# Performance work log

Measured on AMD Instinct MI355X. Metric: run time of the kernel, lower is better.

Reference implementation:

```python
import jax, jax.numpy as jnp
import numpy as np

INPUT_DIM = 1024
HIDDEN_DIM = 1024

def setup_inputs() -> dict:
    key = jax.random.key(0)
    ks = jax.random.split(key, 9)
    s_in = 1.0 / np.sqrt(INPUT_DIM)
    s_h = 1.0 / np.sqrt(HIDDEN_DIM)
    x = jax.random.normal(ks[0], (4, 2048, INPUT_DIM), dtype=jnp.float32)
    Wq = jax.random.uniform(ks[1], (INPUT_DIM, HIDDEN_DIM), jnp.float32, -s_in, s_in)
    bq = jax.random.uniform(ks[2], (HIDDEN_DIM,), jnp.float32, -s_in, s_in)
    Wk = jax.random.uniform(ks[3], (INPUT_DIM, HIDDEN_DIM), jnp.float32, -s_in, s_in)
    bk = jax.random.uniform(ks[4], (HIDDEN_DIM,), jnp.float32, -s_in, s_in)
    Wv = jax.random.uniform(ks[5], (INPUT_DIM, HIDDEN_DIM), jnp.float32, -s_in, s_in)
    bv = jax.random.uniform(ks[6], (HIDDEN_DIM,), jnp.float32, -s_in, s_in)
    Wo = jax.random.uniform(ks[7], (HIDDEN_DIM, INPUT_DIM), jnp.float32, -s_h, s_h)
    bo = jax.random.uniform(ks[8], (INPUT_DIM,), jnp.float32, -s_h, s_h)
    return {"x": x, "Wq": Wq, "bq": bq, "Wk": Wk, "bk": bk, "Wv": Wv, "bv": bv, "Wo": Wo, "bo": bo}

def reference(x, Wq, bq, Wk, bk, Wv, bv, Wo, bo):
    # x: [B, S, D_in]; scale uses x.shape[-1] (faithful to source, which divides by sqrt(input_dim))
    scale = 1.0 / jnp.sqrt(jnp.asarray(x.shape[-1], dtype=x.dtype))
    Q = jnp.einsum('bsd,dh->bsh', x, Wq) + bq
    K = jnp.einsum('bsd,dh->bsh', x, Wk) + bk
    V = jnp.einsum('bsd,dh->bsh', x, Wv) + bv
    scores = jnp.einsum('bqh,bkh->bqk', Q, K) * scale  # [B, S, S]
    attn = jax.nn.softmax(scores, axis=-1)
    ctx = jnp.einsum('bqk,bkh->bqh', attn, V)
    return jnp.einsum('bsh,hd->bsd', ctx, Wo) + bo
```

## Files before the change

kernel.cpp:

```cpp
#include <hip/hip_runtime.h>
#include <hip/hip_bf16.h>

typedef __attribute__((ext_vector_type(8))) short bf16x8;
typedef __attribute__((ext_vector_type(4))) float f32x4;

#define AS1 __attribute__((address_space(1)))
#define AS3 __attribute__((address_space(3)))

__device__ __forceinline__ unsigned short f2bf(float f) {
  unsigned u = __float_as_uint(f);
  u += 0x7fff + ((u >> 16) & 1);
  return (unsigned short)(u >> 16);
}

__device__ __forceinline__ void gload_lds16(const void* g, void* l) {
  __builtin_amdgcn_global_load_lds((const AS1 unsigned int*)g,
                                   (AS3 unsigned int*)l, 16, 0, 0);
}

template <typename OutT, bool BIAS>
__global__ void gemm_bt(const unsigned short* __restrict__ A,
                        const unsigned short* __restrict__ Bt,
                        OutT* __restrict__ C,
                        const float* __restrict__ bias,
                        int M, int N, int Kd,
                        int lda, int ldb, int ldc,
                        long sA, long sB, long sC,
                        float scale) {
  __shared__ unsigned short ldsA[128 * 32];
  __shared__ unsigned short ldsB[128 * 32];
  const int bz = blockIdx.z;
  A  += (size_t)bz * sA + (size_t)blockIdx.x * 128 * lda;
  Bt += (size_t)bz * sB + (size_t)blockIdx.y * 128 * ldb;

  const int tid  = threadIdx.x;
  const int wave = tid >> 6;
  const int lane = tid & 63;
  const int wm   = (wave >> 1) * 64;
  const int wn   = (wave & 1) * 64;
  const int quad = lane >> 4;
  const int l16  = lane & 15;
  const int srow = wave * 16 + (lane >> 2);
  const int scol = (lane & 3) * 8;

  f32x4 acc[4][4] = {};

  for (int k0 = 0; k0 < Kd; k0 += 32) {
    __syncthreads();
    gload_lds16(A  + (size_t)srow * lda + k0 + scol,        (char*)ldsA + wave * 1024);
    gload_lds16(A  + (size_t)(srow + 64) * lda + k0 + scol, (char*)ldsA + 4096 + wave * 1024);
    gload_lds16(Bt + (size_t)srow * ldb + k0 + scol,        (char*)ldsB + wave * 1024);
    gload_lds16(Bt + (size_t)(srow + 64) * ldb + k0 + scol, (char*)ldsB + 4096 + wave * 1024);
    __syncthreads();

    bf16x8 af[4], bfr[4];
#pragma unroll
    for (int i = 0; i < 4; ++i)
      af[i] = *(const bf16x8*)&ldsA[(wm + i * 16 + l16) * 32 + quad * 8];
#pragma unroll
    for (int j = 0; j < 4; ++j)
      bfr[j] = *(const bf16x8*)&ldsB[(wn + j * 16 + l16) * 32 + quad * 8];
#pragma unroll
    for (int i = 0; i < 4; ++i)
#pragma unroll
      for (int j = 0; j < 4; ++j)
        acc[i][j] = __builtin_amdgcn_mfma_f32_16x16x32_bf16(af[i], bfr[j], acc[i][j], 0, 0, 0);
  }

  const int row0 = blockIdx.x * 128 + wm;
  const int col0 = blockIdx.y * 128 + wn;
  C += (size_t)bz * sC;
#pragma unroll
  for (int i = 0; i < 4; ++i) {
#pragma unroll
    for (int j = 0; j < 4; ++j) {
      const int col = col0 + j * 16 + l16;
      const float bv = BIAS ? bias[col] : 0.0f;
#pragma unroll
      for (int r = 0; r < 4; ++r) {
        const int row = row0 + i * 16 + quad * 4 + r;
        const float v = acc[i][j][r] * scale + bv;
        if constexpr (sizeof(OutT) == 4)
          C[(size_t)row * ldc + col] = v;
        else
          C[(size_t)row * ldc + col] = (OutT)f2bf(v);
      }
    }
  }
}

__global__ void cvt_x(const float* __restrict__ in, unsigned short* __restrict__ out, int n4) {
  const int i = blockIdx.x * blockDim.x + threadIdx.x;
  if (i < n4) {
    const float4 v = ((const float4*)in)[i];
    uint2 o;
    o.x = (unsigned)f2bf(v.x) | ((unsigned)f2bf(v.y) << 16);
    o.y = (unsigned)f2bf(v.z) | ((unsigned)f2bf(v.w) << 16);
    ((uint2*)out)[i] = o;
  }
}

__global__ void cvtT_w(const float* __restrict__ in, unsigned short* __restrict__ out,
                       int rows, int cols) {
  __shared__ unsigned short tile[64][65];
  const int r0 = blockIdx.y * 64, c0 = blockIdx.x * 64;
  for (int i = threadIdx.y; i < 64; i += 4)
    tile[i][threadIdx.x] = f2bf(in[(size_t)(r0 + i) * cols + c0 + threadIdx.x]);
  __syncthreads();
  for (int i = threadIdx.y; i < 64; i += 4)
    out[(size_t)(c0 + i) * rows + r0 + threadIdx.x] = tile[threadIdx.x][i];
}

__global__ void transpose_bf16(const unsigned short* __restrict__ in,
                               unsigned short* __restrict__ out, int rows, int cols) {
  __shared__ unsigned short tile[64][65];
  const int b = blockIdx.z;
  in  += (size_t)b * rows * cols;
  out += (size_t)b * rows * cols;
  const int r0 = blockIdx.y * 64, c0 = blockIdx.x * 64;
  for (int i = threadIdx.y; i < 64; i += 4)
    tile[i][threadIdx.x] = in[(size_t)(r0 + i) * cols + c0 + threadIdx.x];
  __syncthreads();
  for (int i = threadIdx.y; i < 64; i += 4)
    out[(size_t)(c0 + i) * rows + r0 + threadIdx.x] = tile[threadIdx.x][i];
}

__global__ __launch_bounds__(256) void softmax_inplace(float* __restrict__ scores) {
  float* p = scores + (size_t)blockIdx.x * 2048;
  const int t = threadIdx.x;
  float4 v0 = ((const float4*)p)[t * 2];
  float4 v1 = ((const float4*)p)[t * 2 + 1];

  float m = fmaxf(fmaxf(fmaxf(v0.x, v0.y), fmaxf(v0.z, v0.w)),
                  fmaxf(fmaxf(v1.x, v1.y), fmaxf(v1.z, v1.w)));
#pragma unroll
  for (int off = 32; off; off >>= 1) m = fmaxf(m, __shfl_xor(m, off, 64));

  __shared__ float red[4];
  __shared__ float bcast[2];
  const int wave = t >> 6, lane = t & 63;
  if (lane == 0) red[wave] = m;
  __syncthreads();
  if (t == 0) bcast[0] = fmaxf(fmaxf(red[0], red[1]), fmaxf(red[2], red[3]));
  __syncthreads();
  m = bcast[0];

  v0.x = __expf(v0.x - m); v0.y = __expf(v0.y - m);
  v0.z = __expf(v0.z - m); v0.w = __expf(v0.w - m);
  v1.x = __expf(v1.x - m); v1.y = __expf(v1.y - m);
  v1.z = __expf(v1.z - m); v1.w = __expf(v1.w - m);

  float s = v0.x + v0.y + v0.z + v0.w + v1.x + v1.y + v1.z + v1.w;
#pragma unroll
  for (int off = 32; off; off >>= 1) s += __shfl_xor(s, off, 64);
  if (lane == 0) red[wave] = s;
  __syncthreads();
  if (t == 0) bcast[1] = red[0] + red[1] + red[2] + red[3];
  __syncthreads();
  const float inv = 1.0f / bcast[1];

  uint4 ov;
  ov.x = (unsigned)f2bf(v0.x * inv) | ((unsigned)f2bf(v0.y * inv) << 16);
  ov.y = (unsigned)f2bf(v0.z * inv) | ((unsigned)f2bf(v0.w * inv) << 16);
  ov.z = (unsigned)f2bf(v1.x * inv) | ((unsigned)f2bf(v1.y * inv) << 16);
  ov.w = (unsigned)f2bf(v1.z * inv) | ((unsigned)f2bf(v1.w * inv) << 16);
  ((uint4*)p)[t] = ov;
}

extern "C" void kernel_launch(void* const* d_in, const int* in_sizes, int n_in,
                              void* d_out, int out_size, void* d_ws, size_t ws_size,
                              hipStream_t stream) {
  const float* x  = (const float*)d_in[0];
  const float* Wq = (const float*)d_in[1];
  const float* bq = (const float*)d_in[2];
  const float* Wk = (const float*)d_in[3];
  const float* bk = (const float*)d_in[4];
  const float* Wv = (const float*)d_in[5];
  const float* bv = (const float*)d_in[6];
  const float* Wo = (const float*)d_in[7];
  const float* bo = (const float*)d_in[8];
  float* out = (float*)d_out;

  char* ws = (char*)d_ws;
  const size_t XB = 8192UL * 1024 * 2;
  const size_t WB = 1024UL * 1024 * 2;
  unsigned short* xb   = (unsigned short*)(ws);
  unsigned short* Wqb  = (unsigned short*)(ws + XB);
  unsigned short* Wkb  = (unsigned short*)(ws + XB + WB);
  unsigned short* Wvb  = (unsigned short*)(ws + XB + 2 * WB);
  unsigned short* Wob  = (unsigned short*)(ws + XB + 3 * WB);
  unsigned short* Qb   = (unsigned short*)(ws + XB + 4 * WB);
  unsigned short* Kb   = (unsigned short*)(ws + 2 * XB + 4 * WB);
  unsigned short* Vb   = (unsigned short*)(ws + 3 * XB + 4 * WB);
  unsigned short* Vtb  = (unsigned short*)(ws + 4 * XB + 4 * WB);
  unsigned short* ctxb = (unsigned short*)(ws + 5 * XB + 4 * WB);
  float*          sc   = (float*)(ws + 6 * XB + 4 * WB);

  const dim3 blk(256);

  cvt_x<<<2097152 / 256, 256, 0, stream>>>(x, xb, 2097152);
  cvtT_w<<<dim3(16, 16), dim3(64, 4), 0, stream>>>(Wq, Wqb, 1024, 1024);
  cvtT_w<<<dim3(16, 16), dim3(64, 4), 0, stream>>>(Wk, Wkb, 1024, 1024);
  cvtT_w<<<dim3(16, 16), dim3(64, 4), 0, stream>>>(Wv, Wvb, 1024, 1024);
  cvtT_w<<<dim3(16, 16), dim3(64, 4), 0, stream>>>(Wo, Wob, 1024, 1024);

  gemm_bt<unsigned short, true><<<dim3(64, 8, 1), blk, 0, stream>>>(
      xb, Wqb, Qb, bq, 8192, 1024, 1024, 1024, 1024, 1024, 0, 0, 0, 1.0f);
  gemm_bt<unsigned short, true><<<dim3(64, 8, 1), blk, 0, stream>>>(
      xb, Wkb, Kb, bk, 8192, 1024, 1024, 1024, 1024, 1024, 0, 0, 0, 1.0f);
  gemm_bt<unsigned short, true><<<dim3(64, 8, 1), blk, 0, stream>>>(
      xb, Wvb, Vb, bv, 8192, 1024, 1024, 1024, 1024, 1024, 0, 0, 0, 1.0f);

  transpose_bf16<<<dim3(16, 32, 4), dim3(64, 4), 0, stream>>>(Vb, Vtb, 2048, 1024);

  gemm_bt<float, false><<<dim3(16, 16, 4), blk, 0, stream>>>(
      Qb, Kb, sc, nullptr, 2048, 2048, 1024, 1024, 1024, 2048,
      2048L * 1024, 2048L * 1024, 2048L * 2048, 0.03125f);

  softmax_inplace<<<8192, 256, 0, stream>>>(sc);

  gemm_bt<unsigned short, false><<<dim3(16, 8, 4), blk, 0, stream>>>(
      (unsigned short*)sc, Vtb, ctxb, nullptr, 2048, 1024, 2048, 4096, 2048, 1024,
      2048L * 4096, 1024L * 2048, 2048L * 1024, 1.0f);

  gemm_bt<float, true><<<dim3(64, 8, 1), blk, 0, stream>>>(
      ctxb, Wob, out, bo, 8192, 1024, 1024, 1024, 1024, 1024, 0, 0, 0, 1.0f);
}
```

Baseline: 348.8 us.

## Fuse QKV projections into one GEMM, swizzle LDS, narrow N tiles for small GEMMs

Concatenates Wq/Wk/Wv and their biases so a single GEMM with N=3072 produces an interleaved QKV buffer, which the score GEMM and V transpose then read through strides. Adds an XOR swizzle to the global-to-LDS column mapping and the fragment reads to reduce LDS bank conflicts. Templates the GEMM on N-tile width and uses 64-wide tiles for the ctx and output GEMMs to launch more blocks. Adds three small device-to-device memcpys for the biases and reads strided QKV rows.

```diff
diff --git a/kernel.cpp b/kernel.cpp
--- a/kernel.cpp
+++ b/kernel.cpp
@@ -18,62 +18,65 @@
                                    (AS3 unsigned int*)l, 16, 0, 0);
 }
 
-template <typename OutT, bool BIAS>
-__global__ void gemm_bt(const unsigned short* __restrict__ A,
-                        const unsigned short* __restrict__ Bt,
-                        OutT* __restrict__ C,
-                        const float* __restrict__ bias,
-                        int M, int N, int Kd,
-                        int lda, int ldb, int ldc,
-                        long sA, long sB, long sC,
-                        float scale) {
+template <typename OutT, bool BIAS, int NJ>
+__global__ __launch_bounds__(256) void gemm_bt(
+    const unsigned short* __restrict__ A,
+    const unsigned short* __restrict__ Bt,
+    OutT* __restrict__ C,
+    const float* __restrict__ bias,
+    int Kd, int lda, int ldb, int ldc,
+    long sA, long sB, long sC,
+    float scale) {
+  constexpr int TN = NJ * 32;
   __shared__ unsigned short ldsA[128 * 32];
-  __shared__ unsigned short ldsB[128 * 32];
+  __shared__ unsigned short ldsB[TN * 32];
   const int bz = blockIdx.z;
   A  += (size_t)bz * sA + (size_t)blockIdx.x * 128 * lda;
-  Bt += (size_t)bz * sB + (size_t)blockIdx.y * 128 * ldb;
+  Bt += (size_t)bz * sB + (size_t)blockIdx.y * TN * ldb;
 
   const int tid  = threadIdx.x;
   const int wave = tid >> 6;
   const int lane = tid & 63;
   const int wm   = (wave >> 1) * 64;
-  const int wn   = (wave & 1) * 64;
+  const int wn   = (wave & 1) * (NJ * 16);
   const int quad = lane >> 4;
   const int l16  = lane & 15;
   const int srow = wave * 16 + (lane >> 2);
-  const int scol = (lane & 3) * 8;
-
-  f32x4 acc[4][4] = {};
+  const int cg   = ((lane & 3) ^ ((lane >> 2) & 3) ^ (lane >> 4)) * 8;
+  const int prd  = (quad ^ (l16 & 3) ^ ((l16 >> 2) & 3)) * 8;
+
+  f32x4 acc[4][NJ] = {};
 
   for (int k0 = 0; k0 < Kd; k0 += 32) {
     __syncthreads();
-    gload_lds16(A  + (size_t)srow * lda + k0 + scol,        (char*)ldsA + wave * 1024);
-    gload_lds16(A  + (size_t)(srow + 64) * lda + k0 + scol, (char*)ldsA + 4096 + wave * 1024);
-    gload_lds16(Bt + (size_t)srow * ldb + k0 + scol,        (char*)ldsB + wave * 1024);
-    gload_lds16(Bt + (size_t)(srow + 64) * ldb + k0 + scol, (char*)ldsB + 4096 + wave * 1024);
+    gload_lds16(A + (size_t)srow * lda + k0 + cg,        (char*)ldsA + wave * 1024);
+    gload_lds16(A + (size_t)(srow + 64) * lda + k0 + cg, (char*)ldsA + 4096 + wave * 1024);
+#pragma unroll
+    for (int n = 0; n < TN; n += 64)
+      gload_lds16(Bt + (size_t)(srow + n) * ldb + k0 + cg, (char*)ldsB + n * 64 + wave * 1024);
     __syncthreads();
 
-    bf16x8 af[4], bfr[4];
+    bf16x8 af[4], bfr[NJ];
 #pragma unroll
     for (int i = 0; i < 4; ++i)
-      af[i] = *(const bf16x8*)&ldsA[(wm + i * 16 + l16) * 32 + quad * 8];
-#pragma unroll
-    for (int j = 0; j < 4; ++j)
-      bfr[j] = *(const bf16x8*)&ldsB[(wn + j * 16 + l16) * 32 + quad * 8];
+      af[i] = *(const bf16x8*)&ldsA[(wm + i * 16 + l16) * 32 + prd];
+#pragma unroll
+    for (int j = 0; j < NJ; ++j)
+      bfr[j] = *(const bf16x8*)&ldsB[(wn + j * 16 + l16) * 32 + prd];
 #pragma unroll
     for (int i = 0; i < 4; ++i)
 #pragma unroll
-      for (int j = 0; j < 4; ++j)
+      for (int j = 0; j < NJ; ++j)
         acc[i][j] = __builtin_amdgcn_mfma_f32_16x16x32_bf16(af[i], bfr[j], acc[i][j], 0, 0, 0);
   }
 
   const int row0 = blockIdx.x * 128 + wm;
-  const int col0 = blockIdx.y * 128 + wn;
+  const int col0 = blockIdx.y * TN + wn;
   C += (size_t)bz * sC;
 #pragma unroll
   for (int i = 0; i < 4; ++i) {
 #pragma unroll
-    for (int j = 0; j < 4; ++j) {
+    for (int j = 0; j < NJ; ++j) {
       const int col = col0 + j * 16 + l16;
       const float bv = BIAS ? bias[col] : 0.0f;
 #pragma unroll
@@ -112,17 +115,19 @@
 }
 
 __global__ void transpose_bf16(const unsigned short* __restrict__ in,
-                               unsigned short* __restrict__ out, int rows, int cols) {
+                               unsigned short* __restrict__ out,
+                               int rows, int ld_in, long sIn,
+                               int cols_out_rows , long sOut) {
   __shared__ unsigned short tile[64][65];
   const int b = blockIdx.z;
-  in  += (size_t)b * rows * cols;
-  out += (size_t)b * rows * cols;
+  in  += (size_t)b * sIn;
+  out += (size_t)b * sOut;
   const int r0 = blockIdx.y * 64, c0 = blockIdx.x * 64;
   for (int i = threadIdx.y; i < 64; i += 4)
-    tile[i][threadIdx.x] = in[(size_t)(r0 + i) * cols + c0 + threadIdx.x];
-  __syncthreads();
-  for (int i = threadIdx.y; i < 64; i += 4)
-    out[(size_t)(c0 + i) * rows + r0 + threadIdx.x] = tile[threadIdx.x][i];
+    tile[i][threadIdx.x] = in[(size_t)(r0 + i) * ld_in + c0 + threadIdx.x];
+  __syncthreads();
+  for (int i = threadIdx.y; i < 64; i += 4)
+    out[(size_t)(c0 + i) * cols_out_rows + r0 + threadIdx.x] = tile[threadIdx.x][i];
 }
 
 __global__ __launch_bounds__(256) void softmax_inplace(float* __restrict__ scores) {
@@ -182,47 +187,44 @@
   float* out = (float*)d_out;
 
   char* ws = (char*)d_ws;
-  const size_t XB = 8192UL * 1024 * 2;
-  const size_t WB = 1024UL * 1024 * 2;
-  unsigned short* xb   = (unsigned short*)(ws);
-  unsigned short* Wqb  = (unsigned short*)(ws + XB);
-  unsigned short* Wkb  = (unsigned short*)(ws + XB + WB);
-  unsigned short* Wvb  = (unsigned short*)(ws + XB + 2 * WB);
-  unsigned short* Wob  = (unsigned short*)(ws + XB + 3 * WB);
-  unsigned short* Qb   = (unsigned short*)(ws + XB + 4 * WB);
-  unsigned short* Kb   = (unsigned short*)(ws + 2 * XB + 4 * WB);
-  unsigned short* Vb   = (unsigned short*)(ws + 3 * XB + 4 * WB);
-  unsigned short* Vtb  = (unsigned short*)(ws + 4 * XB + 4 * WB);
-  unsigned short* ctxb = (unsigned short*)(ws + 5 * XB + 4 * WB);
-  float*          sc   = (float*)(ws + 6 * XB + 4 * WB);
+  size_t off = 0;
+  auto alloc = [&](size_t bytes) { char* p = ws + off; off += (bytes + 255) & ~255UL; return p; };
+  unsigned short* xb    = (unsigned short*)alloc(8192UL * 1024 * 2);
+  unsigned short* Wqkvb = (unsigned short*)alloc(3072UL * 1024 * 2);
+  unsigned short* Wob   = (unsigned short*)alloc(1024UL * 1024 * 2);
+  float*          bqkv  = (float*)alloc(3072UL * 4);
+  unsigned short* qkv   = (unsigned short*)alloc(8192UL * 3072 * 2);
+  unsigned short* Vtb   = (unsigned short*)alloc(4UL * 1024 * 2048 * 2);
+  unsigned short* ctxb  = (unsigned short*)alloc(8192UL * 1024 * 2);
+  float*          sc    = (float*)alloc(4UL * 2048 * 2048 * 4);
 
   const dim3 blk(256);
 
   cvt_x<<<2097152 / 256, 256, 0, stream>>>(x, xb, 2097152);
-  cvtT_w<<<dim3(16, 16), dim3(64, 4), 0, stream>>>(Wq, Wqb, 1024, 1024);
-  cvtT_w<<<dim3(16, 16), dim3(64, 4), 0, stream>>>(Wk, Wkb, 1024, 1024);
-  cvtT_w<<<dim3(16, 16), dim3(64, 4), 0, stream>>>(Wv, Wvb, 1024, 1024);
+  cvtT_w<<<dim3(16, 16), dim3(64, 4), 0, stream>>>(Wq, Wqkvb, 1024, 1024);
+  cvtT_w<<<dim3(16, 16), dim3(64, 4), 0, stream>>>(Wk, Wqkvb + 1024 * 1024, 1024, 1024);
+  cvtT_w<<<dim3(16, 16), dim3(64, 4), 0, stream>>>(Wv, Wqkvb + 2048 * 1024, 1024, 1024);
   cvtT_w<<<dim3(16, 16), dim3(64, 4), 0, stream>>>(Wo, Wob, 1024, 1024);
-
-  gemm_bt<unsigned short, true><<<dim3(64, 8, 1), blk, 0, stream>>>(
-      xb, Wqb, Qb, bq, 8192, 1024, 1024, 1024, 1024, 1024, 0, 0, 0, 1.0f);
-  gemm_bt<unsigned short, true><<<dim3(64, 8, 1), blk, 0, stream>>>(
-      xb, Wkb, Kb, bk, 8192, 1024, 1024, 1024, 1024, 1024, 0, 0, 0, 1.0f);
-  gemm_bt<unsigned short, true><<<dim3(64, 8, 1), blk, 0, stream>>>(
-      xb, Wvb, Vb, bv, 8192, 1024, 1024, 1024, 1024, 1024, 0, 0, 0, 1.0f);
-
-  transpose_bf16<<<dim3(16, 32, 4), dim3(64, 4), 0, stream>>>(Vb, Vtb, 2048, 1024);
-
-  gemm_bt<float, false><<<dim3(16, 16, 4), blk, 0, stream>>>(
-      Qb, Kb, sc, nullptr, 2048, 2048, 1024, 1024, 1024, 2048,
-      2048L * 1024, 2048L * 1024, 2048L * 2048, 0.03125f);
+  hipMemcpyAsync(bqkv,        bq, 1024 * 4, hipMemcpyDeviceToDevice, stream);
+  hipMemcpyAsync(bqkv + 1024, bk, 1024 * 4, hipMemcpyDeviceToDevice, stream);
+  hipMemcpyAsync(bqkv + 2048, bv, 1024 * 4, hipMemcpyDeviceToDevice, stream);
+
+  gemm_bt<unsigned short, true, 4><<<dim3(64, 24, 1), blk, 0, stream>>>(
+      xb, Wqkvb, qkv, bqkv, 1024, 1024, 1024, 3072, 0, 0, 0, 1.0f);
+
+  transpose_bf16<<<dim3(16, 32, 4), dim3(64, 4), 0, stream>>>(
+      qkv + 2048, Vtb, 2048, 3072, 2048L * 3072, 2048, 1024L * 2048);
+
+  gemm_bt<float, false, 4><<<dim3(16, 16, 4), blk, 0, stream>>>(
+      qkv, qkv + 1024, sc, nullptr, 1024, 3072, 3072, 2048,
+      2048L * 3072, 2048L * 3072, 2048L * 2048, 0.03125f);
 
   softmax_inplace<<<8192, 256, 0, stream>>>(sc);
 
-  gemm_bt<unsigned short, false><<<dim3(16, 8, 4), blk, 0, stream>>>(
-      (unsigned short*)sc, Vtb, ctxb, nullptr, 2048, 1024, 2048, 4096, 2048, 1024,
+  gemm_bt<unsigned short, false, 2><<<dim3(16, 16, 4), blk, 0, stream>>>(
+      (unsigned short*)sc, Vtb, ctxb, nullptr, 2048, 4096, 2048, 1024,
       2048L * 4096, 1024L * 2048, 2048L * 1024, 1.0f);
 
-  gemm_bt<float, true><<<dim3(64, 8, 1), blk, 0, stream>>>(
-      ctxb, Wob, out, bo, 8192, 1024, 1024, 1024, 1024, 1024, 0, 0, 0, 1.0f);
-}
+  gemm_bt<float, true, 2><<<dim3(64, 16, 1), blk, 0, stream>>>(
+      ctxb, Wob, out, bo, 1024, 1024, 1024, 1024, 0, 0, 0, 1.0f);
+}
```

After: 374.5 us. 7.4% more time.
